# Optimization experiments

Hardware: AMD Instinct MI355X
Metric: run time of the kernel (lower is better)

## Reference

```python
import jax, jax.numpy as jnp
import numpy as np
from jax.ops import segment_sum

N_IN, N_OUT, E = 100000, 50000, 1600000
IN_CH, OUT_CH, K = 32, 64, 4
K3 = K * K * K


def setup_inputs() -> dict:
    key = jax.random.key(0)
    ks = jax.random.split(key, 8)
    feats = jax.random.normal(ks[0], (N_IN, IN_CH), jnp.float32)
    inp_points = jax.random.uniform(ks[1], (N_IN, 3), dtype=jnp.float32)
    out_points = jax.random.uniform(ks[2], (N_OUT, 3), dtype=jnp.float32)
    out_extents = jnp.ones((1,), jnp.float32) * 0.2  # voxel size
    scale_compat = jax.random.uniform(ks[3], (E,), dtype=jnp.float32)
    neighbors_index = jax.random.randint(ks[4], (E,), 0, N_IN, jnp.int32)
    rs = jnp.sort(jax.random.randint(ks[5], (N_OUT + 1,), 0, E, jnp.int32))
    neighbors_row_splits = rs.at[0].set(0).at[-1].set(E)
    neighbors_distance = jax.random.uniform(ks[6], (E,), dtype=jnp.float32)
    W = jax.random.normal(ks[7], (K, K, K, IN_CH, OUT_CH), jnp.float32) * 0.05
    b = jnp.zeros((OUT_CH,), jnp.float32)
    return dict(feats=feats, inp_points=inp_points, out_points=out_points,
                out_extents=out_extents, scale_compat=scale_compat,
                neighbors_index=neighbors_index,
                neighbors_row_splits=neighbors_row_splits,
                neighbors_distance=neighbors_distance, W=W, b=b)


def window_poly6(r):
    # poly6 smoothing window on normalized distance r in [0,1]
    return jnp.clip((1.0 - r * r) ** 3, 0.0, 1.0)


def _cconv(feats, inp_points, out_points, out_extents, imp,
           neighbors_index, neighbors_row_splits, W, b):
    n_out = out_points.shape[0]
    e = neighbors_index.shape[0]
    # CSR row_splits -> destination (output point) id per edge
    out_id = jnp.searchsorted(neighbors_row_splits,
                              jnp.arange(e, dtype=neighbors_row_splits.dtype),
                              side='right') - 1
    out_id = jnp.clip(out_id, 0, n_out - 1)
    # relative position normalized to [-1,1] ball by the voxel extent
    rel = (inp_points[neighbors_index] - out_points[out_id]) * (2.0 / out_extents[0])
    r = jnp.linalg.norm(rel, axis=1, keepdims=True)
    inf = jnp.max(jnp.abs(rel), axis=1, keepdims=True)
    # ball_to_cube_radial: stretch along ray so unit sphere -> unit cube surface
    scale = jnp.where(inf > 1e-8, r / jnp.maximum(inf, 1e-8), 0.0)
    u = jnp.clip(rel * scale, -1.0, 1.0)
    # trilinear (align-corners) filter coordinates in [0, K-1]
    t = (u + 1.0) * (0.5 * (K - 1))
    f = jnp.clip(jnp.floor(t), 0.0, K - 2.0)
    frac = t - f
    fi = f.astype(jnp.int32)
    fw = feats[neighbors_index] * imp[:, None]          # [E, C_in]
    # accumulate importance-weighted features into (output point, kernel bin)
    A = jnp.zeros((n_out * K3, fw.shape[1]), fw.dtype)
    for dx in (0, 1):
        wx = frac[:, 0] if dx else 1.0 - frac[:, 0]
        for dy in (0, 1):
            wy = frac[:, 1] if dy else 1.0 - frac[:, 1]
            for dz in (0, 1):
                wz = frac[:, 2] if dz else 1.0 - frac[:, 2]
                w = wx * wy * wz
                kbin = ((fi[:, 0] + dx) * K + fi[:, 1] + dy) * K + fi[:, 2] + dz
                seg = out_id * K3 + kbin
                A = A + segment_sum(fw * w[:, None], seg, num_segments=n_out * K3)
    A = A.reshape(n_out, K3, -1)                         # [N_out, K^3, C_in]
    y = jnp.einsum('jki,kio->jo', A, W.reshape(K3, fw.shape[1], -1))
    # normalize=True: divide by summed neighbor importance
    denom = segment_sum(imp, out_id, num_segments=n_out)
    y = y / jnp.where(denom != 0, denom, 1.0)[:, None]
    return jax.nn.relu(y + b)


def reference(feats, inp_points, out_points, out_extents, scale_compat,
              neighbors_index, neighbors_row_splits, neighbors_distance, W, b):
    imp = scale_compat * window_poly6(neighbors_distance)
    return _cconv(feats, inp_points, out_points, out_extents, imp,
                  neighbors_index, neighbors_row_splits, W, b)
```

## Files before the change

### kernel.cpp

```cpp
#include <hip/hip_runtime.h>

#define G 8
#define THREADS 512
#define IN_CH 32
#define OUT_CH 64
#define KK 4
#define K3 64
#define CHUNK 256

__global__ __launch_bounds__(THREADS, 4) void cconv_fused_kernel(
    const float* __restrict__ feats,
    const float* __restrict__ inp_points,
    const float* __restrict__ out_points,
    const float* __restrict__ out_extents,
    const float* __restrict__ scale_compat,
    const int*   __restrict__ nbr_index,
    const int*   __restrict__ row_splits,
    const float* __restrict__ nbr_dist,
    const float* __restrict__ Wmat,
    const float* __restrict__ bias,
    float* __restrict__ out,
    int n_out)
{
    __shared__ float A_s[G * K3 * IN_CH];
    __shared__ float den_s[G];
    __shared__ unsigned int mask_s[G][2];
    __shared__ int   rs_s[G + 1];
    __shared__ float opts_s[G * 3];
    __shared__ int   st_nbr[CHUNK];
    __shared__ float st_imp[CHUNK];
    __shared__ float st_frx[CHUNK];
    __shared__ float st_fry[CHUNK];
    __shared__ float st_frz[CHUNK];
    __shared__ int   st_bg[CHUNK];

    const int tid  = threadIdx.x;
    const int g0   = blockIdx.x * G;
    const int lane = tid & 63;

    {
        float4* A4z = (float4*)A_s;
        #pragma unroll
        for (int i = 0; i < 8; ++i)
            A4z[tid + i * THREADS] = make_float4(0.f, 0.f, 0.f, 0.f);
    }
    if (tid < G) { den_s[tid] = 0.f; mask_s[tid][0] = 0u; mask_s[tid][1] = 0u; }
    if (tid <= G) {
        int gg = g0 + tid;
        if (gg > n_out) gg = n_out;
        rs_s[tid] = row_splits[gg];
    }
    if (tid < G * 3) {
        int gg = g0 + tid / 3;
        opts_s[tid] = (gg < n_out) ? out_points[gg * 3 + tid % 3] : 0.f;
    }
    __syncthreads();

    const float inv_ext = 2.0f / out_extents[0];
    int rsl[G + 1];
    #pragma unroll
    for (int t = 0; t <= G; ++t) rsl[t] = rs_s[t];
    const int e0 = rsl[0], e1 = rsl[G];

    const int slot = tid >> 5;
    const int c    = tid & 31;

    for (int ch0 = e0; ch0 < e1; ch0 += CHUNK) {
        const int rem = e1 - ch0;
        const int nch = rem < CHUNK ? rem : CHUNK;

        int          eg   = -1;
        float        eimp = 0.f;
        unsigned int em_lo = 0u, em_hi = 0u;
        if (tid < nch) {
            const int   e   = ch0 + tid;
            const int   nbr = nbr_index[e];
            const float sc  = scale_compat[e];
            const float dd  = nbr_dist[e];
            float p = 1.f - dd * dd;
            p = p * p * p;
            p = fminf(fmaxf(p, 0.f), 1.f);
            const float imp = sc * p;

            int g = 0;
            #pragma unroll
            for (int t = 1; t < G; ++t) g += (e >= rsl[t]) ? 1 : 0;

            const float rx = (inp_points[nbr * 3 + 0] - opts_s[g * 3 + 0]) * inv_ext;
            const float ry = (inp_points[nbr * 3 + 1] - opts_s[g * 3 + 1]) * inv_ext;
            const float rz = (inp_points[nbr * 3 + 2] - opts_s[g * 3 + 2]) * inv_ext;

            const float r   = sqrtf(rx * rx + ry * ry + rz * rz);
            const float inf = fmaxf(fabsf(rx), fmaxf(fabsf(ry), fabsf(rz)));
            const float scl = (inf > 1e-8f) ? (r / fmaxf(inf, 1e-8f)) : 0.f;

            const float ux = fminf(fmaxf(rx * scl, -1.f), 1.f);
            const float uy = fminf(fmaxf(ry * scl, -1.f), 1.f);
            const float uz = fminf(fmaxf(rz * scl, -1.f), 1.f);

            const float tx = (ux + 1.f) * 1.5f;
            const float ty = (uy + 1.f) * 1.5f;
            const float tz = (uz + 1.f) * 1.5f;

            const float fx = fminf(fmaxf(floorf(tx), 0.f), 2.f);
            const float fy = fminf(fmaxf(floorf(ty), 0.f), 2.f);
            const float fz = fminf(fmaxf(floorf(tz), 0.f), 2.f);

            const float frx = tx - fx, fry = ty - fy, frz = tz - fz;
            const int ix = (int)fx, iy = (int)fy, iz = (int)fz;
            const int base = (ix * KK + iy) * KK + iz;

            st_nbr[tid] = nbr;
            st_imp[tid] = imp;
            st_frx[tid] = frx;
            st_fry[tid] = fry;
            st_frz[tid] = frz;
            st_bg[tid]  = base | (g << 8);

            const float wx0 = 1.f - frx, wx1 = frx;
            const float wy0 = 1.f - fry, wy1 = fry;
            const float wz0 = 1.f - frz, wz1 = frz;
            #define MB(OFF, WV) { if ((WV) > 0.f) { const int k = base + (OFF); \
                if (k < 32) em_lo |= (1u << k); else em_hi |= (1u << (k - 32)); } }
            MB(0,  wx0 * wy0 * wz0) MB(1,  wx0 * wy0 * wz1)
            MB(4,  wx0 * wy1 * wz0) MB(5,  wx0 * wy1 * wz1)
            MB(16, wx1 * wy0 * wz0) MB(17, wx1 * wy0 * wz1)
            MB(20, wx1 * wy1 * wz0) MB(21, wx1 * wy1 * wz1)
            #undef MB
            eg = g; eimp = imp;
        }
        if (tid < CHUNK) {
            #pragma unroll
            for (int d = 1; d < 64; d <<= 1) {
                const float        oi = __shfl_up(eimp, d);
                const unsigned int ol = __shfl_up(em_lo, d);
                const unsigned int oh = __shfl_up(em_hi, d);
                const int          og = __shfl_up(eg, d);
                if (lane >= d && og == eg) { eimp += oi; em_lo |= ol; em_hi |= oh; }
            }
            const int gnext = __shfl_down(eg, 1);
            const bool tail = (lane == 63) || (gnext != eg);
            if (tail && eg >= 0) {
                atomicAdd(&den_s[eg], eimp);
                if (em_lo) atomicOr(&mask_s[eg][0], em_lo);
                if (em_hi) atomicOr(&mask_s[eg][1], em_hi);
            }
        }
        __syncthreads();

        #define SCAT(I, FV) { const int i = (I); if (i < nch) {               \
            const float imp = st_imp[i];                                      \
            const float frx = st_frx[i], fry = st_fry[i], frz = st_frz[i];    \
            const int bg = st_bg[i];                                          \
            const int g = bg >> 8; const int base = bg & 0xff;                \
            const float fwc = (FV) * imp;                                     \
            const float wx0 = 1.f - frx, wx1 = frx;                           \
            const float wy0 = 1.f - fry, wy1 = fry;                           \
            const float wz0 = 1.f - frz, wz1 = frz;                           \
            float* Ab = &A_s[(((g << 6) + base) << 5) + c]; float w;          \
            w = wx0 * wy0 * wz0; if (w > 0.f) atomicAdd(Ab + (0  << 5), fwc * w); \
            w = wx0 * wy0 * wz1; if (w > 0.f) atomicAdd(Ab + (1  << 5), fwc * w); \
            w = wx0 * wy1 * wz0; if (w > 0.f) atomicAdd(Ab + (4  << 5), fwc * w); \
            w = wx0 * wy1 * wz1; if (w > 0.f) atomicAdd(Ab + (5  << 5), fwc * w); \
            w = wx1 * wy0 * wz0; if (w > 0.f) atomicAdd(Ab + (16 << 5), fwc * w); \
            w = wx1 * wy0 * wz1; if (w > 0.f) atomicAdd(Ab + (17 << 5), fwc * w); \
            w = wx1 * wy1 * wz0; if (w > 0.f) atomicAdd(Ab + (20 << 5), fwc * w); \
            w = wx1 * wy1 * wz1; if (w > 0.f) atomicAdd(Ab + (21 << 5), fwc * w); } }

        float fv0, fv1, fv2, fv3;
        {
            const int i0 = slot, i1 = slot + 16, i2 = slot + 32, i3 = slot + 48;
            fv0 = (i0 < nch) ? feats[st_nbr[i0] * IN_CH + c] : 0.f;
            fv1 = (i1 < nch) ? feats[st_nbr[i1] * IN_CH + c] : 0.f;
            fv2 = (i2 < nch) ? feats[st_nbr[i2] * IN_CH + c] : 0.f;
            fv3 = (i3 < nch) ? feats[st_nbr[i3] * IN_CH + c] : 0.f;
        }
        for (int bi = 0; bi < nch; bi += 64) {
            const int ni = bi + 64;
            float nf0 = 0.f, nf1 = 0.f, nf2 = 0.f, nf3 = 0.f;
            if (ni < nch) {
                const int i0 = ni + slot, i1 = ni + slot + 16,
                          i2 = ni + slot + 32, i3 = ni + slot + 48;
                nf0 = (i0 < nch) ? feats[st_nbr[i0] * IN_CH + c] : 0.f;
                nf1 = (i1 < nch) ? feats[st_nbr[i1] * IN_CH + c] : 0.f;
                nf2 = (i2 < nch) ? feats[st_nbr[i2] * IN_CH + c] : 0.f;
                nf3 = (i3 < nch) ? feats[st_nbr[i3] * IN_CH + c] : 0.f;
            }
            SCAT(bi + slot,      fv0)
            SCAT(bi + slot + 16, fv1)
            SCAT(bi + slot + 32, fv2)
            SCAT(bi + slot + 48, fv3)
            fv0 = nf0; fv1 = nf1; fv2 = nf2; fv3 = nf3;
        }
        #undef SCAT
        __syncthreads();
    }

    const int wave = tid >> 6;
    const int o4   = lane & 15;
    const int i4   = lane >> 4;

    const unsigned int mlo = __builtin_amdgcn_readfirstlane(mask_s[wave][0]);
    const unsigned int mhi = __builtin_amdgcn_readfirstlane(mask_s[wave][1]);
    unsigned long long m = ((unsigned long long)mhi << 32) | mlo;

    float4 acc0 = make_float4(0.f, 0.f, 0.f, 0.f);
    float4 acc1 = make_float4(0.f, 0.f, 0.f, 0.f);
    float4 acc2 = make_float4(0.f, 0.f, 0.f, 0.f);
    float4 acc3 = make_float4(0.f, 0.f, 0.f, 0.f);

    const float4* __restrict__ W4 = (const float4*)Wmat;
    const float*  __restrict__ Ag = &A_s[(wave * K3) * IN_CH];

    float4 wA[8];
    float4 wB[8];

    #define LOADW(P, K) { const float4* Wk = &W4[(((K) << 5) + (i4 << 3)) * 16 + o4]; \
        P[0] = Wk[0];  P[1] = Wk[16]; P[2] = Wk[32]; P[3] = Wk[48];                    \
        P[4] = Wk[64]; P[5] = Wk[80]; P[6] = Wk[96]; P[7] = Wk[112]; }

    #define DOFMA(P, K) {                                                     \
        const float4 a0 = *(const float4*)&Ag[((K) << 5) + (i4 << 3)];        \
        const float4 a1 = *(const float4*)&Ag[((K) << 5) + (i4 << 3) + 4];    \
        acc0.x = fmaf(a0.x, P[0].x, acc0.x); acc0.y = fmaf(a0.x, P[0].y, acc0.y); \
        acc0.z = fmaf(a0.x, P[0].z, acc0.z); acc0.w = fmaf(a0.x, P[0].w, acc0.w); \
        acc1.x = fmaf(a0.y, P[1].x, acc1.x); acc1.y = fmaf(a0.y, P[1].y, acc1.y); \
        acc1.z = fmaf(a0.y, P[1].z, acc1.z); acc1.w = fmaf(a0.y, P[1].w, acc1.w); \
        acc2.x = fmaf(a0.z, P[2].x, acc2.x); acc2.y = fmaf(a0.z, P[2].y, acc2.y); \
        acc2.z = fmaf(a0.z, P[2].z, acc2.z); acc2.w = fmaf(a0.z, P[2].w, acc2.w); \
        acc3.x = fmaf(a0.w, P[3].x, acc3.x); acc3.y = fmaf(a0.w, P[3].y, acc3.y); \
        acc3.z = fmaf(a0.w, P[3].z, acc3.z); acc3.w = fmaf(a0.w, P[3].w, acc3.w); \
        acc0.x = fmaf(a1.x, P[4].x, acc0.x); acc0.y = fmaf(a1.x, P[4].y, acc0.y); \
        acc0.z = fmaf(a1.x, P[4].z, acc0.z); acc0.w = fmaf(a1.x, P[4].w, acc0.w); \
        acc1.x = fmaf(a1.y, P[5].x, acc1.x); acc1.y = fmaf(a1.y, P[5].y, acc1.y); \
        acc1.z = fmaf(a1.y, P[5].z, acc1.z); acc1.w = fmaf(a1.y, P[5].w, acc1.w); \
        acc2.x = fmaf(a1.z, P[6].x, acc2.x); acc2.y = fmaf(a1.z, P[6].y, acc2.y); \
        acc2.z = fmaf(a1.z, P[6].z, acc2.z); acc2.w = fmaf(a1.z, P[6].w, acc2.w); \
        acc3.x = fmaf(a1.w, P[7].x, acc3.x); acc3.y = fmaf(a1.w, P[7].y, acc3.y); \
        acc3.z = fmaf(a1.w, P[7].z, acc3.z); acc3.w = fmaf(a1.w, P[7].w, acc3.w); }

    int kA = -1, kB = -1;
    if (m) { kA = __ffsll(m) - 1; m &= m - 1; LOADW(wA, kA) }
    while (kA >= 0) {
        kB = -1;
        if (m) { kB = __ffsll(m) - 1; m &= m - 1; LOADW(wB, kB) }
        DOFMA(wA, kA)
        if (kB < 0) break;
        kA = -1;
        if (m) { kA = __ffsll(m) - 1; m &= m - 1; LOADW(wA, kA) }
        DOFMA(wB, kB)
    }
    #undef LOADW
    #undef DOFMA

    float4 t;
    t.x = (acc0.x + acc1.x) + (acc2.x + acc3.x);
    t.y = (acc0.y + acc1.y) + (acc2.y + acc3.y);
    t.z = (acc0.z + acc1.z) + (acc2.z + acc3.z);
    t.w = (acc0.w + acc1.w) + (acc2.w + acc3.w);

    t.x += __shfl_xor(t.x, 16); t.y += __shfl_xor(t.y, 16);
    t.z += __shfl_xor(t.z, 16); t.w += __shfl_xor(t.w, 16);
    t.x += __shfl_xor(t.x, 32); t.y += __shfl_xor(t.y, 32);
    t.z += __shfl_xor(t.z, 32); t.w += __shfl_xor(t.w, 32);

    const int row = g0 + wave;
    if (lane < 16 && row < n_out) {
        float d = den_s[wave];
        d = (d != 0.f) ? d : 1.f;
        const float inv_d = 1.f / d;
        const float4 b4 = ((const float4*)bias)[o4];
        float4 y;
        y.x = fmaxf(t.x * inv_d + b4.x, 0.f);
        y.y = fmaxf(t.y * inv_d + b4.y, 0.f);
        y.z = fmaxf(t.z * inv_d + b4.z, 0.f);
        y.w = fmaxf(t.w * inv_d + b4.w, 0.f);
        ((float4*)out)[row * 16 + o4] = y;
    }
}

extern "C" void kernel_launch(void* const* d_in, const int* in_sizes, int n_in,
                              void* d_out, int out_size, void* d_ws, size_t ws_size,
                              hipStream_t stream) {
    const float* feats        = (const float*)d_in[0];
    const float* inp_points   = (const float*)d_in[1];
    const float* out_points   = (const float*)d_in[2];
    const float* out_extents  = (const float*)d_in[3];
    const float* scale_compat = (const float*)d_in[4];
    const int*   nbr_index    = (const int*)d_in[5];
    const int*   row_splits   = (const int*)d_in[6];
    const float* nbr_dist     = (const float*)d_in[7];
    const float* Wmat         = (const float*)d_in[8];
    const float* bias         = (const float*)d_in[9];
    float*       out          = (float*)d_out;

    const int n_out = in_sizes[2] / 3;
    if (n_out <= 0) return;
    const int nwg = (n_out + G - 1) / G;

    hipLaunchKernelGGL(cconv_fused_kernel, dim3(nwg), dim3(THREADS), 0, stream,
                       feats, inp_points, out_points, out_extents, scale_compat,
                       nbr_index, row_splits, nbr_dist, Wmat, bias, out, n_out);
}
```

Before: 669.0 us.

## Issue all feature gathers before edge geometry and iterate nonzero trilinear corners

At the top of each chunk, every thread now loads all 16 of its neighbor feature values straight from global memory, using nbr_index directly instead of the staged shared-memory index. This lets the gather latency overlap the per-edge geometry computation and the scan. The geometry step also packs an 8-bit mask of corners with nonzero weight into st_bg, and the scatter loop visits only those corners with ffs. The cost is 16 live registers per thread plus extra nbr_index reads, which may hurt occupancy under the 4-block launch bound, and the corner loop adds divergent control flow.

```diff
diff --git a/kernel.cpp b/kernel.cpp
--- a/kernel.cpp
+++ b/kernel.cpp
@@ -3,12 +3,11 @@
 #define G 8
 #define THREADS 512
 #define IN_CH 32
-#define OUT_CH 64
 #define KK 4
 #define K3 64
 #define CHUNK 256
 
-__global__ __launch_bounds__(THREADS, 4) void cconv_fused_kernel(
+__global__ __launch_bounds__(THREADS, 4) void cconv_kern(
     const float* __restrict__ feats,
     const float* __restrict__ inp_points,
     const float* __restrict__ out_points,
@@ -27,7 +26,6 @@
     __shared__ unsigned int mask_s[G][2];
     __shared__ int   rs_s[G + 1];
     __shared__ float opts_s[G * 3];
-    __shared__ int   st_nbr[CHUNK];
     __shared__ float st_imp[CHUNK];
     __shared__ float st_frx[CHUNK];
     __shared__ float st_fry[CHUNK];
@@ -68,6 +66,15 @@
     for (int ch0 = e0; ch0 < e1; ch0 += CHUNK) {
         const int rem = e1 - ch0;
         const int nch = rem < CHUNK ? rem : CHUNK;
+
+        #define PREF(VAR, M) float VAR = 0.f; { const int i = slot + ((M) << 4);   \
+            if (i < nch) { const int nb = nbr_index[ch0 + i];                      \
+                           VAR = feats[nb * IN_CH + c]; } }
+        PREF(f00, 0)  PREF(f01, 1)  PREF(f02, 2)  PREF(f03, 3)
+        PREF(f04, 4)  PREF(f05, 5)  PREF(f06, 6)  PREF(f07, 7)
+        PREF(f08, 8)  PREF(f09, 9)  PREF(f10, 10) PREF(f11, 11)
+        PREF(f12, 12) PREF(f13, 13) PREF(f14, 14) PREF(f15, 15)
+        #undef PREF
 
         int          eg   = -1;
         float        eimp = 0.f;
@@ -110,23 +117,25 @@
             const int ix = (int)fx, iy = (int)fy, iz = (int)fz;
             const int base = (ix * KK + iy) * KK + iz;
 
-            st_nbr[tid] = nbr;
+            const float wx0 = 1.f - frx, wx1 = frx;
+            const float wy0 = 1.f - fry, wy1 = fry;
+            const float wz0 = 1.f - frz, wz1 = frz;
+
+            int cmask = 0;
+            #define MB(J, OFF, WV) { if ((WV) > 0.f) { cmask |= (1 << (J));      \
+                const int k = base + (OFF);                                      \
+                if (k < 32) em_lo |= (1u << k); else em_hi |= (1u << (k - 32)); } }
+            MB(0, 0,  wx0 * wy0 * wz0) MB(1, 1,  wx0 * wy0 * wz1)
+            MB(2, 4,  wx0 * wy1 * wz0) MB(3, 5,  wx0 * wy1 * wz1)
+            MB(4, 16, wx1 * wy0 * wz0) MB(5, 17, wx1 * wy0 * wz1)
+            MB(6, 20, wx1 * wy1 * wz0) MB(7, 21, wx1 * wy1 * wz1)
+            #undef MB
+
             st_imp[tid] = imp;
             st_frx[tid] = frx;
             st_fry[tid] = fry;
             st_frz[tid] = frz;
-            st_bg[tid]  = base | (g << 8);
-
-            const float wx0 = 1.f - frx, wx1 = frx;
-            const float wy0 = 1.f - fry, wy1 = fry;
-            const float wz0 = 1.f - frz, wz1 = frz;
-            #define MB(OFF, WV) { if ((WV) > 0.f) { const int k = base + (OFF); \
-                if (k < 32) em_lo |= (1u << k); else em_hi |= (1u << (k - 32)); } }
-            MB(0,  wx0 * wy0 * wz0) MB(1,  wx0 * wy0 * wz1)
-            MB(4,  wx0 * wy1 * wz0) MB(5,  wx0 * wy1 * wz1)
-            MB(16, wx1 * wy0 * wz0) MB(17, wx1 * wy0 * wz1)
-            MB(20, wx1 * wy1 * wz0) MB(21, wx1 * wy1 * wz1)
-            #undef MB
+            st_bg[tid]  = base | (g << 8) | (cmask << 16);
             eg = g; eimp = imp;
         }
         if (tid < CHUNK) {
@@ -148,50 +157,29 @@
         }
         __syncthreads();
 
-        #define SCAT(I, FV) { const int i = (I); if (i < nch) {               \
-            const float imp = st_imp[i];                                      \
-            const float frx = st_frx[i], fry = st_fry[i], frz = st_frz[i];    \
-            const int bg = st_bg[i];                                          \
-            const int g = bg >> 8; const int base = bg & 0xff;                \
-            const float fwc = (FV) * imp;                                     \
-            const float wx0 = 1.f - frx, wx1 = frx;                           \
-            const float wy0 = 1.f - fry, wy1 = fry;                           \
-            const float wz0 = 1.f - frz, wz1 = frz;                           \
-            float* Ab = &A_s[(((g << 6) + base) << 5) + c]; float w;          \
-            w = wx0 * wy0 * wz0; if (w > 0.f) atomicAdd(Ab + (0  << 5), fwc * w); \
-            w = wx0 * wy0 * wz1; if (w > 0.f) atomicAdd(Ab + (1  << 5), fwc * w); \
-            w = wx0 * wy1 * wz0; if (w > 0.f) atomicAdd(Ab + (4  << 5), fwc * w); \
-            w = wx0 * wy1 * wz1; if (w > 0.f) atomicAdd(Ab + (5  << 5), fwc * w); \
-            w = wx1 * wy0 * wz0; if (w > 0.f) atomicAdd(Ab + (16 << 5), fwc * w); \
-            w = wx1 * wy0 * wz1; if (w > 0.f) atomicAdd(Ab + (17 << 5), fwc * w); \
-            w = wx1 * wy1 * wz0; if (w > 0.f) atomicAdd(Ab + (20 << 5), fwc * w); \
-            w = wx1 * wy1 * wz1; if (w > 0.f) atomicAdd(Ab + (21 << 5), fwc * w); } }
-
-        float fv0, fv1, fv2, fv3;
-        {
-            const int i0 = slot, i1 = slot + 16, i2 = slot + 32, i3 = slot + 48;
-            fv0 = (i0 < nch) ? feats[st_nbr[i0] * IN_CH + c] : 0.f;
-            fv1 = (i1 < nch) ? feats[st_nbr[i1] * IN_CH + c] : 0.f;
-            fv2 = (i2 < nch) ? feats[st_nbr[i2] * IN_CH + c] : 0.f;
-            fv3 = (i3 < nch) ? feats[st_nbr[i3] * IN_CH + c] : 0.f;
-        }
-        for (int bi = 0; bi < nch; bi += 64) {
-            const int ni = bi + 64;
-            float nf0 = 0.f, nf1 = 0.f, nf2 = 0.f, nf3 = 0.f;
-            if (ni < nch) {
-                const int i0 = ni + slot, i1 = ni + slot + 16,
-                          i2 = ni + slot + 32, i3 = ni + slot + 48;
-                nf0 = (i0 < nch) ? feats[st_nbr[i0] * IN_CH + c] : 0.f;
-                nf1 = (i1 < nch) ? feats[st_nbr[i1] * IN_CH + c] : 0.f;
-                nf2 = (i2 < nch) ? feats[st_nbr[i2] * IN_CH + c] : 0.f;
-                nf3 = (i3 < nch) ? feats[st_nbr[i3] * IN_CH + c] : 0.f;
-            }
-            SCAT(bi + slot,      fv0)
-            SCAT(bi + slot + 16, fv1)
-            SCAT(bi + slot + 32, fv2)
-            SCAT(bi + slot + 48, fv3)
-            fv0 = nf0; fv1 = nf1; fv2 = nf2; fv3 = nf3;
-        }
+        #define SCAT(M, FV) { const int i = slot + ((M) << 4); if (i < nch) {     \
+            const float imp = st_imp[i];                                          \
+            const float frx = st_frx[i], fry = st_fry[i], frz = st_frz[i];        \
+            const int bg = st_bg[i];                                              \
+            const int g = (bg >> 8) & 0xff; const int base = bg & 0xff;           \
+            int cm = (bg >> 16) & 0xff;                                           \
+            const float fwc = (FV) * imp;                                         \
+            const float wx0 = 1.f - frx, wx1 = frx;                               \
+            const float wy0 = 1.f - fry, wy1 = fry;                               \
+            const float wz0 = 1.f - frz, wz1 = frz;                               \
+            float* Ab = &A_s[(((g << 6) + base) << 5) + c];                       \
+            while (cm) {                                                          \
+                const int j = __ffs(cm) - 1; cm &= cm - 1;                        \
+                const float w = ((j & 4) ? wx1 : wx0) *                           \
+                                ((j & 2) ? wy1 : wy0) *                           \
+                                ((j & 1) ? wz1 : wz0);                            \
+                const int off = ((j & 4) << 2) | ((j & 2) << 1) | (j & 1);        \
+                atomicAdd(Ab + (off << 5), fwc * w);                              \
+            } } }
+        SCAT(0,  f00) SCAT(1,  f01) SCAT(2,  f02) SCAT(3,  f03)
+        SCAT(4,  f04) SCAT(5,  f05) SCAT(6,  f06) SCAT(7,  f07)
+        SCAT(8,  f08) SCAT(9,  f09) SCAT(10, f10) SCAT(11, f11)
+        SCAT(12, f12) SCAT(13, f13) SCAT(14, f14) SCAT(15, f15)
         #undef SCAT
         __syncthreads();
     }
@@ -298,7 +286,7 @@
     if (n_out <= 0) return;
     const int nwg = (n_out + G - 1) / G;
 
-    hipLaunchKernelGGL(cconv_fused_kernel, dim3(nwg), dim3(THREADS), 0, stream,
+    hipLaunchKernelGGL(cconv_kern, dim3(nwg), dim3(THREADS), 0, stream,
                        feats, inp_points, out_points, out_extents, scale_compat,
                        nbr_index, row_splits, nbr_dist, Wmat, bias, out, n_out);
 }
```

After: 726.4 us. 8.6% more time.

## Halve output points per block and split kernel bins across two waves

Applied to the files above, without the earlier changes.

Each block now handles 4 output points instead of 8, with two waves per point. Each wave covers half of the 64 kernel bins using a 32-bit occupancy mask, and the two partial results are reduced through shared memory before the bias, normalization and ReLU epilogue. This cuts shared memory per block, which may allow more resident blocks, and spreads the dense matmul across more waves. The cost is twice as many blocks, so the per-block setup and the edge-scatter phase are repeated more often, plus an extra synchronization and reduction.

```diff
diff --git a/kernel.cpp b/kernel.cpp
--- a/kernel.cpp
+++ b/kernel.cpp
@@ -1,14 +1,13 @@
 #include <hip/hip_runtime.h>
 
-#define G 8
+#define G 4
 #define THREADS 512
 #define IN_CH 32
-#define OUT_CH 64
 #define KK 4
 #define K3 64
 #define CHUNK 256
 
-__global__ __launch_bounds__(THREADS, 4) void cconv_fused_kernel(
+__global__ __launch_bounds__(THREADS, 4) void cconv_kern(
     const float* __restrict__ feats,
     const float* __restrict__ inp_points,
     const float* __restrict__ out_points,
@@ -28,11 +27,13 @@
     __shared__ int   rs_s[G + 1];
     __shared__ float opts_s[G * 3];
     __shared__ int   st_nbr[CHUNK];
-    __shared__ float st_imp[CHUNK];
-    __shared__ float st_frx[CHUNK];
-    __shared__ float st_fry[CHUNK];
-    __shared__ float st_frz[CHUNK];
+    __shared__ float st_f[4 * CHUNK];
     __shared__ int   st_bg[CHUNK];
+
+    float* const st_imp = st_f;
+    float* const st_frx = st_f + CHUNK;
+    float* const st_fry = st_f + 2 * CHUNK;
+    float* const st_frz = st_f + 3 * CHUNK;
 
     const int tid  = threadIdx.x;
     const int g0   = blockIdx.x * G;
@@ -41,7 +42,7 @@
     {
         float4* A4z = (float4*)A_s;
         #pragma unroll
-        for (int i = 0; i < 8; ++i)
+        for (int i = 0; i < 4; ++i)
             A4z[tid + i * THREADS] = make_float4(0.f, 0.f, 0.f, 0.f);
     }
     if (tid < G) { den_s[tid] = 0.f; mask_s[tid][0] = 0u; mask_s[tid][1] = 0u; }
@@ -196,13 +197,14 @@
         __syncthreads();
     }
 
-    const int wave = tid >> 6;
-    const int o4   = lane & 15;
-    const int i4   = lane >> 4;
-
-    const unsigned int mlo = __builtin_amdgcn_readfirstlane(mask_s[wave][0]);
-    const unsigned int mhi = __builtin_amdgcn_readfirstlane(mask_s[wave][1]);
-    unsigned long long m = ((unsigned long long)mhi << 32) | mlo;
+    const int w   = tid >> 6;
+    const int pg  = w >> 1;
+    const int h   = w & 1;
+    const int o4  = lane & 15;
+    const int i4  = lane >> 4;
+
+    unsigned int m32 = __builtin_amdgcn_readfirstlane(mask_s[pg][h]);
+    const int kofs = h << 5;
 
     float4 acc0 = make_float4(0.f, 0.f, 0.f, 0.f);
     float4 acc1 = make_float4(0.f, 0.f, 0.f, 0.f);
@@ -210,7 +212,7 @@
     float4 acc3 = make_float4(0.f, 0.f, 0.f, 0.f);
 
     const float4* __restrict__ W4 = (const float4*)Wmat;
-    const float*  __restrict__ Ag = &A_s[(wave * K3) * IN_CH];
+    const float*  __restrict__ Ag = &A_s[(pg * K3) * IN_CH];
 
     float4 wA[8];
     float4 wB[8];
@@ -240,14 +242,14 @@
         acc3.z = fmaf(a1.w, P[7].z, acc3.z); acc3.w = fmaf(a1.w, P[7].w, acc3.w); }
 
     int kA = -1, kB = -1;
-    if (m) { kA = __ffsll(m) - 1; m &= m - 1; LOADW(wA, kA) }
+    if (m32) { kA = (__ffs(m32) - 1) + kofs; m32 &= m32 - 1; LOADW(wA, kA) }
     while (kA >= 0) {
         kB = -1;
-        if (m) { kB = __ffsll(m) - 1; m &= m - 1; LOADW(wB, kB) }
+        if (m32) { kB = (__ffs(m32) - 1) + kofs; m32 &= m32 - 1; LOADW(wB, kB) }
         DOFMA(wA, kA)
         if (kB < 0) break;
         kA = -1;
-        if (m) { kA = __ffsll(m) - 1; m &= m - 1; LOADW(wA, kA) }
+        if (m32) { kA = (__ffs(m32) - 1) + kofs; m32 &= m32 - 1; LOADW(wA, kA) }
         DOFMA(wB, kB)
     }
     #undef LOADW
@@ -264,18 +266,21 @@
     t.x += __shfl_xor(t.x, 32); t.y += __shfl_xor(t.y, 32);
     t.z += __shfl_xor(t.z, 32); t.w += __shfl_xor(t.w, 32);
 
-    const int row = g0 + wave;
-    if (lane < 16 && row < n_out) {
-        float d = den_s[wave];
-        d = (d != 0.f) ? d : 1.f;
-        const float inv_d = 1.f / d;
-        const float4 b4 = ((const float4*)bias)[o4];
-        float4 y;
-        y.x = fmaxf(t.x * inv_d + b4.x, 0.f);
-        y.y = fmaxf(t.y * inv_d + b4.y, 0.f);
-        y.z = fmaxf(t.z * inv_d + b4.z, 0.f);
-        y.w = fmaxf(t.w * inv_d + b4.w, 0.f);
-        ((float4*)out)[row * 16 + o4] = y;
+    __syncthreads();
+    if (lane < 16)
+        ((float4*)st_f)[w * 16 + o4] = t;
+    __syncthreads();
+
+    if (tid < G * 64) {
+        const int go = tid >> 6;
+        const int oo = tid & 63;
+        const int row = g0 + go;
+        if (row < n_out) {
+            const float s = st_f[(2 * go) * 64 + oo] + st_f[(2 * go + 1) * 64 + oo];
+            float d = den_s[go];
+            d = (d != 0.f) ? d : 1.f;
+            out[row * 64 + oo] = fmaxf(s / d + bias[oo], 0.f);
+        }
     }
 }
 
@@ -298,7 +303,7 @@
     if (n_out <= 0) return;
     const int nwg = (n_out + G - 1) / G;
 
-    hipLaunchKernelGGL(cconv_fused_kernel, dim3(nwg), dim3(THREADS), 0, stream,
+    hipLaunchKernelGGL(cconv_kern, dim3(nwg), dim3(THREADS), 0, stream,
                        feats, inp_points, out_points, out_extents, scale_compat,
                        nbr_index, row_splits, nbr_dist, Wmat, bias, out, n_out);
 }
```

New measurement: 694.6 us. 1.04x slower.
